# Performance work log

Hardware: AMD Instinct MI355X
Metric: run time of the kernel (lower is better)

The kernel has to match this reference:

```python
import jax, jax.numpy as jnp
import numpy as np

B, N = 8, 16384
DIMS = [3, 64, 128, 1024]  # conv1d(kernel=1) channel sizes: in -> layer_dims -> feat_size
EPS = 1e-5  # BatchNorm1d default eps


def setup_inputs() -> dict:
    key = jax.random.key(0)
    ks = jax.random.split(key, 8)
    inp = {"x": jax.random.normal(ks[0], (B, N, 3), dtype=jnp.float32)}
    for i in range(3):
        cin, cout = DIMS[i], DIMS[i + 1]
        k1, k2 = jax.random.split(ks[i + 1])
        inp[f"W{i}"] = jax.random.normal(k1, (cout, cin), dtype=jnp.float32) * (1.0 / np.sqrt(cin))
        inp[f"b{i}"] = jax.random.normal(k2, (cout,), dtype=jnp.float32) * 0.01
        inp[f"g{i}"] = jnp.ones((cout,), dtype=jnp.float32)   # BN gamma (init 1)
        inp[f"be{i}"] = jnp.zeros((cout,), dtype=jnp.float32)  # BN beta (init 0)
    return inp


def _bn(h, gamma, beta):
    # training-mode BatchNorm1d: stats over batch and point dims, biased variance
    m = h.mean(axis=(0, 1))
    v = h.var(axis=(0, 1))
    return (h - m) * jax.lax.rsqrt(v + EPS) * gamma + beta


def reference(x, W0, b0, g0, be0, W1, b1, g1, be1, W2, b2, g2, be2):
    # pointwise Conv1d (kernel=1) == per-point linear; layout (B, N, C)
    h = jax.nn.relu(_bn(jnp.einsum('bnc,oc->bno', x, W0) + b0, g0, be0))
    local = h  # (B, N, 64) local features
    h = jax.nn.relu(_bn(jnp.einsum('bnc,oc->bno', h, W1) + b1, g1, be1))
    h = _bn(jnp.einsum('bnc,oc->bno', h, W2) + b2, g2, be2)  # no relu on last layer
    gfeat = h.max(axis=1)  # (B, 1024) global max-pool over points
    # concat broadcast global feature with local features -> (B, 1024+64, N) in torch layout
    out = jnp.concatenate(
        [jnp.broadcast_to(gfeat[:, :, None], (B, DIMS[-1], N)), jnp.swapaxes(local, 1, 2)], axis=1)
    return out
```

## Files before the change

kernel.cpp:

```cpp
#include <hip/hip_runtime.h>


#define P_TOT  131072
#define NPTS   16384
#define EPSF   1e-5f

typedef __bf16 bf16x8 __attribute__((ext_vector_type(8)));
typedef float  f32x4  __attribute__((ext_vector_type(4)));

#define H0_OFF   0u
#define H1_OFF   16777216u
#define W1B_OFF  50331648u
#define W2B_OFF  50348032u
#define ST_OFF   50610176u
#define MM_OFF   50662400u

#define S0   0
#define Q0   64
#define S1   128
#define Q1   256
#define S2   384
#define Q2   1408
#define SC0  2432
#define SH0  2496
#define SC1  2560
#define SH1  2688
#define GF   4864
#define STATS_ZERO_N 2432

__device__ __forceinline__ unsigned short f2bf(float f) {
  unsigned u = __builtin_bit_cast(unsigned, f);
  u += 0x7fffu + ((u >> 16) & 1u);
  return (unsigned short)(u >> 16);
}
__device__ __forceinline__ float bf2f(unsigned short s) {
  return __builtin_bit_cast(float, ((unsigned)s) << 16);
}
__device__ __forceinline__ unsigned encf(float f) {
  unsigned u = __builtin_bit_cast(unsigned, f);
  return (u & 0x80000000u) ? ~u : (u | 0x80000000u);
}
__device__ __forceinline__ float decf(unsigned e) {
  unsigned u = (e & 0x80000000u) ? (e & 0x7fffffffu) : ~e;
  return __builtin_bit_cast(float, u);
}
__device__ __forceinline__ uint4 pack8(const float* f) {
  uint4 r;
  r.x = (unsigned)f2bf(f[0]) | ((unsigned)f2bf(f[1]) << 16);
  r.y = (unsigned)f2bf(f[2]) | ((unsigned)f2bf(f[3]) << 16);
  r.z = (unsigned)f2bf(f[4]) | ((unsigned)f2bf(f[5]) << 16);
  r.w = (unsigned)f2bf(f[6]) | ((unsigned)f2bf(f[7]) << 16);
  return r;
}
__device__ __forceinline__ uint4 bnrelu8(uint4 v, const float* sc, const float* sh) {
  unsigned vv[4] = {v.x, v.y, v.z, v.w};
  float f[8];
#pragma unroll
  for (int i = 0; i < 4; ++i) {
    float a = bf2f((unsigned short)(vv[i] & 0xffffu));
    float b = bf2f((unsigned short)(vv[i] >> 16));
    f[2*i]   = fmaxf(fmaf(a, sc[2*i],   sh[2*i]),   0.f);
    f[2*i+1] = fmaxf(fmaf(b, sc[2*i+1], sh[2*i+1]), 0.f);
  }
  return pack8(f);
}

__global__ __launch_bounds__(256) void k_layer0(const float* __restrict__ x,
                                                const float* __restrict__ W0,
                                                const float* __restrict__ W1,
                                                const float* __restrict__ W2,
                                                unsigned short* __restrict__ h0b,
                                                unsigned short* __restrict__ w1b,
                                                unsigned short* __restrict__ w2b,
                                                float* __restrict__ stats,
                                                unsigned* __restrict__ mmx) {
  int t = threadIdx.x;
  if (blockIdx.x >= 2048) {
    int tid = (blockIdx.x - 2048) * 256 + t;
    const int stride = 128 * 256;
    for (int i = tid; i < 1024 * 128; i += stride) w2b[i] = f2bf(W2[i]);
    for (int i = tid; i < 128 * 64;   i += stride) w1b[i] = f2bf(W1[i]);
    for (int i = 128 + tid; i < STATS_ZERO_N; i += stride) stats[i] = 0.f;
    for (int i = tid; i < 8192; i += stride) { mmx[i] = 0u; mmx[8192 + i] = 0xffffffffu; }
    return;
  }
  __shared__ float w0s[192];
  __shared__ float bs[64], bq[64];
  if (t < 192) w0s[t] = W0[t];
  if (t < 64) { bs[t] = 0.f; bq[t] = 0.f; }
  __syncthreads();
  int p  = blockIdx.x * 64 + (t >> 2);
  int cs = (t & 3) * 16;
  float x0 = x[p*3], x1 = x[p*3+1], x2 = x[p*3+2];
  float v[16];
#pragma unroll
  for (int j = 0; j < 16; ++j) {
    int c = cs + j;
    v[j] = x0 * w0s[c*3] + x1 * w0s[c*3+1] + x2 * w0s[c*3+2];
  }
  uint4* dst = (uint4*)(h0b + p*64 + cs);
  dst[0] = pack8(&v[0]);
  dst[1] = pack8(&v[8]);
  int lane = t & 63;
#pragma unroll
  for (int j = 0; j < 16; ++j) {
    float s = v[j], q = v[j]*v[j];
#pragma unroll
    for (int m = 4; m < 64; m <<= 1) { s += __shfl_xor(s, m, 64); q += __shfl_xor(q, m, 64); }
    if (lane < 4) { atomicAdd(&bs[cs + j], s); atomicAdd(&bq[cs + j], q); }
  }
  __syncthreads();
  if (t < 64) { atomicAdd(&stats[S0 + t], bs[t]); atomicAdd(&stats[Q0 + t], bq[t]); }
}

__global__ void k_fin0(const float* __restrict__ g, const float* __restrict__ be,
                       float* __restrict__ stats) {
  int c = threadIdx.x;
  float m = stats[S0 + c] * (1.f / P_TOT);
  float q = stats[Q0 + c] * (1.f / P_TOT);
  float sc = g[c] * rsqrtf(q - m*m + EPSF);
  stats[SC0 + c] = sc;
  stats[SH0 + c] = be[c] - m * sc;
}
__global__ void k_fin1(const float* __restrict__ g, const float* __restrict__ be,
                       float* __restrict__ stats) {
  int c = threadIdx.x;
  float m = stats[S1 + c] * (1.f / P_TOT);
  float q = stats[Q1 + c] * (1.f / P_TOT);
  float sc = g[c] * rsqrtf(q - m*m + EPSF);
  stats[SC1 + c] = sc;
  stats[SH1 + c] = be[c] - m * sc;
}

__global__ __launch_bounds__(512, 2) void k_gemm1(const unsigned short* __restrict__ h0b,
                                                  const unsigned short* __restrict__ w1b,
                                                  unsigned short* __restrict__ h1b,
                                                  float* __restrict__ stats,
                                                  float* __restrict__ out) {
  __shared__ uint4 arrA[128 * 8];
  int t = threadIdx.x, l = t & 63, w = t >> 6;
  int wr = w >> 2, wc = w & 3;
  bf16x8 bfr[2][2];
#pragma unroll
  for (int nn = 0; nn < 2; ++nn)
#pragma unroll
    for (int kk = 0; kk < 2; ++kk) {
      int j  = wc*32 + nn*16 + (l & 15);
      int k0 = kk*32 + (l >> 4) * 8;
      bfr[nn][kk] = __builtin_bit_cast(bf16x8, *(const uint4*)(w1b + j*64 + k0));
    }
  int kc = t & 7;
  float ssc[8], ssh[8];
#pragma unroll
  for (int j = 0; j < 8; ++j) { ssc[j] = stats[SC0 + kc*8 + j]; ssh[j] = stats[SH0 + kc*8 + j]; }
  float runS[2] = {0,0}, runQ[2] = {0,0};
  int pbase0 = blockIdx.x * 256;
  int srow0 = t >> 3, srow1 = 64 + (t >> 3);
  uint4 v0 = *(const uint4*)(h0b + (pbase0 + srow0) * 64 + kc * 8);
  uint4 v1 = *(const uint4*)(h0b + (pbase0 + srow1) * 64 + kc * 8);
  for (int mt = 0; mt < 2; ++mt) {
    int pbase = pbase0 + mt * 128;
    __syncthreads();
    arrA[srow0*8 + (kc ^ (srow0 & 7))] = bnrelu8(v0, ssc, ssh);
    arrA[srow1*8 + (kc ^ (srow1 & 7))] = bnrelu8(v1, ssc, ssh);
    __syncthreads();
    if (mt == 0) {
      v0 = *(const uint4*)(h0b + (pbase0 + 128 + srow0) * 64 + kc * 8);
      v1 = *(const uint4*)(h0b + (pbase0 + 128 + srow1) * 64 + kc * 8);
    }
    f32x4 acc[4][2];
#pragma unroll
    for (int mm = 0; mm < 4; ++mm)
#pragma unroll
      for (int nn = 0; nn < 2; ++nn) acc[mm][nn] = (f32x4){0.f,0.f,0.f,0.f};
#pragma unroll
    for (int kk = 0; kk < 2; ++kk) {
      bf16x8 a[4];
#pragma unroll
      for (int mm = 0; mm < 4; ++mm) {
        int r  = wr*64 + mm*16 + (l & 15);
        int ck = kk*4 + (l >> 4);
        a[mm] = __builtin_bit_cast(bf16x8, arrA[r*8 + (ck ^ (r & 7))]);
      }
#pragma unroll
      for (int mm = 0; mm < 4; ++mm)
#pragma unroll
        for (int nn = 0; nn < 2; ++nn)
          acc[mm][nn] = __builtin_amdgcn_mfma_f32_16x16x32_bf16(a[mm], bfr[nn][kk], acc[mm][nn], 0, 0, 0);
    }
#pragma unroll
    for (int mm = 0; mm < 4; ++mm) {
      int prow = pbase + wr*64 + mm*16 + (l >> 4) * 4;
#pragma unroll
      for (int nn = 0; nn < 2; ++nn) {
        int col = wc*32 + nn*16 + (l & 15);
#pragma unroll
        for (int r = 0; r < 4; ++r) {
          float f = acc[mm][nn][r];
          h1b[(size_t)(prow + r) * 128 + col] = f2bf(f);
          runS[nn] += f;
          runQ[nn] = fmaf(f, f, runQ[nn]);
        }
      }
    }
    {
      int b  = pbase >> 14;
      int n0 = pbase & 16383;
      int c  = t >> 3;
      int seg = t & 7;
      const unsigned short* lds16 = (const unsigned short*)arrA;
      size_t obase = ((size_t)b * 1088 + 1024 + c) * NPTS + n0 + seg * 16;
#pragma unroll
      for (int q = 0; q < 4; ++q) {
        float f[4];
#pragma unroll
        for (int e = 0; e < 4; ++e) {
          int row = seg*16 + q*4 + e;
          f[e] = bf2f(lds16[(row*8 + ((c >> 3) ^ (row & 7)))*8 + (c & 7)]);
        }
        f32x4 o = {f[0], f[1], f[2], f[3]};
        __builtin_nontemporal_store(o, (f32x4*)(out + obase + q*4));
      }
    }
  }
#pragma unroll
  for (int nn = 0; nn < 2; ++nn) {
    float s = runS[nn], q = runQ[nn];
    s += __shfl_xor(s, 16, 64); s += __shfl_xor(s, 32, 64);
    q += __shfl_xor(q, 16, 64); q += __shfl_xor(q, 32, 64);
    if (l < 16) {
      int col = wc*32 + nn*16 + l;
      atomicAdd(&stats[S1 + col], s);
      atomicAdd(&stats[Q1 + col], q);
    }
  }
}

__global__ __launch_bounds__(512, 2) void k_gemm2(const unsigned short* __restrict__ h1b,
                                                  const unsigned short* __restrict__ w2b,
                                                  float* __restrict__ stats,
                                                  unsigned* __restrict__ mmx) {
  __shared__ uint4 arrA[64 * 16];
  int t = threadIdx.x, l = t & 63, w = t >> 6;
  int jw = blockIdx.x * 256 + w * 32;
  int pbase0 = blockIdx.y * 512;
  int bidx = pbase0 >> 14;
  bf16x8 bfr[2][4];
#pragma unroll
  for (int nn = 0; nn < 2; ++nn)
#pragma unroll
    for (int kk = 0; kk < 4; ++kk) {
      int j  = jw + nn*16 + (l & 15);
      int k0 = kk*32 + (l >> 4) * 8;
      bfr[nn][kk] = __builtin_bit_cast(bf16x8, *(const uint4*)(w2b + j*128 + k0));
    }
  int kc = t & 15;
  float ssc[8], ssh[8];
#pragma unroll
  for (int j = 0; j < 8; ++j) { ssc[j] = stats[SC1 + kc*8 + j]; ssh[j] = stats[SH1 + kc*8 + j]; }
  float runS[2] = {0,0}, runQ[2] = {0,0};
  float runMax[2] = {-3.4e38f, -3.4e38f}, runMin[2] = {3.4e38f, 3.4e38f};
  int srow0 = t >> 4, srow1 = 32 + (t >> 4);
  uint4 v0 = *(const uint4*)(h1b + (size_t)(pbase0 + srow0) * 128 + kc * 8);
  uint4 v1 = *(const uint4*)(h1b + (size_t)(pbase0 + srow1) * 128 + kc * 8);
  for (int mt = 0; mt < 8; ++mt) {
    __syncthreads();
    arrA[srow0*16 + (kc ^ (srow0 & 7))] = bnrelu8(v0, ssc, ssh);
    arrA[srow1*16 + (kc ^ (srow1 & 7))] = bnrelu8(v1, ssc, ssh);
    __syncthreads();
    if (mt < 7) {
      int pb = pbase0 + (mt + 1) * 64;
      v0 = *(const uint4*)(h1b + (size_t)(pb + srow0) * 128 + kc * 8);
      v1 = *(const uint4*)(h1b + (size_t)(pb + srow1) * 128 + kc * 8);
    }
    f32x4 acc[4][2];
#pragma unroll
    for (int mm = 0; mm < 4; ++mm)
#pragma unroll
      for (int nn = 0; nn < 2; ++nn) acc[mm][nn] = (f32x4){0.f,0.f,0.f,0.f};
#pragma unroll
    for (int kk = 0; kk < 4; ++kk) {
      bf16x8 a[4];
#pragma unroll
      for (int mm = 0; mm < 4; ++mm) {
        int r  = mm*16 + (l & 15);
        int ck = kk*4 + (l >> 4);
        a[mm] = __builtin_bit_cast(bf16x8, arrA[r*16 + (ck ^ (r & 7))]);
      }
#pragma unroll
      for (int mm = 0; mm < 4; ++mm)
#pragma unroll
        for (int nn = 0; nn < 2; ++nn)
          acc[mm][nn] = __builtin_amdgcn_mfma_f32_16x16x32_bf16(a[mm], bfr[nn][kk], acc[mm][nn], 0, 0, 0);
    }
#pragma unroll
    for (int nn = 0; nn < 2; ++nn)
#pragma unroll
      for (int mm = 0; mm < 4; ++mm)
#pragma unroll
        for (int r = 0; r < 4; ++r) {
          float f = acc[mm][nn][r];
          runS[nn] += f;
          runQ[nn] = fmaf(f, f, runQ[nn]);
          runMax[nn] = fmaxf(runMax[nn], f);
          runMin[nn] = fminf(runMin[nn], f);
        }
  }
#pragma unroll
  for (int nn = 0; nn < 2; ++nn) {
    float s = runS[nn], q = runQ[nn], mx = runMax[nn], mn = runMin[nn];
    s += __shfl_xor(s, 16, 64); s += __shfl_xor(s, 32, 64);
    q += __shfl_xor(q, 16, 64); q += __shfl_xor(q, 32, 64);
    mx = fmaxf(mx, __shfl_xor(mx, 16, 64)); mx = fmaxf(mx, __shfl_xor(mx, 32, 64));
    mn = fminf(mn, __shfl_xor(mn, 16, 64)); mn = fminf(mn, __shfl_xor(mn, 32, 64));
    if (l < 16) {
      int col = jw + nn*16 + l;
      atomicAdd(&stats[S2 + col], s);
      atomicAdd(&stats[Q2 + col], q);
      atomicMax(&mmx[bidx * 1024 + col], encf(mx));
      atomicMin(&mmx[8192 + bidx * 1024 + col], encf(mn));
    }
  }
}

__global__ void k_fin2(const float* __restrict__ g, const float* __restrict__ be,
                       float* __restrict__ stats, const unsigned* __restrict__ mmx) {
  int idx = blockIdx.x * 256 + threadIdx.x;
  int c = idx & 1023, b = idx >> 10;
  float m = stats[S2 + c] * (1.f / P_TOT);
  float q = stats[Q2 + c] * (1.f / P_TOT);
  float sc = g[c] * rsqrtf(q - m*m + EPSF);
  float sh = be[c] - m * sc;
  float mx = decf(mmx[b * 1024 + c]);
  float mn = decf(mmx[8192 + b * 1024 + c]);
  stats[GF + idx] = (sc >= 0.f) ? fmaf(mx, sc, sh) : fmaf(mn, sc, sh);
}

__global__ __launch_bounds__(256) void k_bcast(const float* __restrict__ stats,
                                               float* __restrict__ out) {
  const float* gf = stats + GF;
  int t = threadIdx.x;
#pragma unroll
  for (int rr = 0; rr < 4; ++rr) {
    int row = blockIdx.x * 4 + rr;
    int b = row >> 10, c = row & 1023;
    float v = gf[row];
    f32x4 o = {v, v, v, v};
    float* base = out + ((size_t)b * 1088 + c) * NPTS;
#pragma unroll
    for (int j = 0; j < 16; ++j)
      __builtin_nontemporal_store(o, (f32x4*)(base + (j * 256 + t) * 4));
  }
}

extern "C" void kernel_launch(void* const* d_in, const int* in_sizes, int n_in,
                              void* d_out, int out_size, void* d_ws, size_t ws_size,
                              hipStream_t stream) {
  const float* x   = (const float*)d_in[0];
  const float* W0  = (const float*)d_in[1];
  const float* g0  = (const float*)d_in[3];
  const float* be0 = (const float*)d_in[4];
  const float* W1  = (const float*)d_in[5];
  const float* g1  = (const float*)d_in[7];
  const float* be1 = (const float*)d_in[8];
  const float* W2  = (const float*)d_in[9];
  const float* g2  = (const float*)d_in[11];
  const float* be2 = (const float*)d_in[12];
  float* out = (float*)d_out;
  char* ws = (char*)d_ws;
  unsigned short* h0b = (unsigned short*)(ws + H0_OFF);
  unsigned short* h1b = (unsigned short*)(ws + H1_OFF);
  unsigned short* w1b = (unsigned short*)(ws + W1B_OFF);
  unsigned short* w2b = (unsigned short*)(ws + W2B_OFF);
  float* stats = (float*)(ws + ST_OFF);
  unsigned* mmx = (unsigned*)(ws + MM_OFF);

  k_layer0<<<2176, 256, 0, stream>>>(x, W0, W1, W2, h0b, w1b, w2b, stats, mmx);
  k_fin0  <<<1, 64, 0, stream>>>(g0, be0, stats);
  k_gemm1 <<<512, 512, 0, stream>>>(h0b, w1b, h1b, stats, out);
  k_fin1  <<<1, 128, 0, stream>>>(g1, be1, stats);
  k_gemm2 <<<dim3(4, 256), 512, 0, stream>>>(h1b, w2b, stats, mmx);
  k_fin2  <<<32, 256, 0, stream>>>(g2, be2, stats, mmx);
  k_bcast <<<2048, 256, 0, stream>>>(stats, out);
}
```

Before: 729.4 us.

## Fold BN finalize kernels into consumer kernels and double gemm2 per-block rows

Removes the three tiny BN-finalize launches by having each consumer block compute scale and shift from the raw sums into shared memory, or per row in the broadcast kernel. Separately, gemm2 blocks now cover 1024 points instead of 512, halving the grid along y and doubling loop iterations. The sync placement moves from the top of each loop iteration to the end. This cuts launch gaps and per-block weight-fragment reloads, at the cost of redundant per-block stat computation and fewer blocks in gemm2.

```diff
diff --git a/kernel.cpp b/kernel.cpp
--- a/kernel.cpp
+++ b/kernel.cpp
@@ -21,11 +21,6 @@
 #define Q1   256
 #define S2   384
 #define Q2   1408
-#define SC0  2432
-#define SH0  2496
-#define SC1  2560
-#define SH1  2688
-#define GF   4864
 #define STATS_ZERO_N 2432
 
 __device__ __forceinline__ unsigned short f2bf(float f) {
@@ -113,33 +108,24 @@
   if (t < 64) { atomicAdd(&stats[S0 + t], bs[t]); atomicAdd(&stats[Q0 + t], bq[t]); }
 }
 
-__global__ void k_fin0(const float* __restrict__ g, const float* __restrict__ be,
-                       float* __restrict__ stats) {
-  int c = threadIdx.x;
-  float m = stats[S0 + c] * (1.f / P_TOT);
-  float q = stats[Q0 + c] * (1.f / P_TOT);
-  float sc = g[c] * rsqrtf(q - m*m + EPSF);
-  stats[SC0 + c] = sc;
-  stats[SH0 + c] = be[c] - m * sc;
-}
-__global__ void k_fin1(const float* __restrict__ g, const float* __restrict__ be,
-                       float* __restrict__ stats) {
-  int c = threadIdx.x;
-  float m = stats[S1 + c] * (1.f / P_TOT);
-  float q = stats[Q1 + c] * (1.f / P_TOT);
-  float sc = g[c] * rsqrtf(q - m*m + EPSF);
-  stats[SC1 + c] = sc;
-  stats[SH1 + c] = be[c] - m * sc;
-}
-
 __global__ __launch_bounds__(512, 2) void k_gemm1(const unsigned short* __restrict__ h0b,
                                                   const unsigned short* __restrict__ w1b,
                                                   unsigned short* __restrict__ h1b,
                                                   float* __restrict__ stats,
-                                                  float* __restrict__ out) {
+                                                  float* __restrict__ out,
+                                                  const float* __restrict__ g0,
+                                                  const float* __restrict__ be0) {
   __shared__ uint4 arrA[128 * 8];
+  __shared__ float sc0s[64], sh0s[64];
   int t = threadIdx.x, l = t & 63, w = t >> 6;
   int wr = w >> 2, wc = w & 3;
+  if (t < 64) {
+    float m = stats[S0 + t] * (1.f / P_TOT);
+    float q = stats[Q0 + t] * (1.f / P_TOT);
+    float sc = g0[t] * rsqrtf(q - m*m + EPSF);
+    sc0s[t] = sc;
+    sh0s[t] = be0[t] - m * sc;
+  }
   bf16x8 bfr[2][2];
 #pragma unroll
   for (int nn = 0; nn < 2; ++nn)
@@ -150,17 +136,17 @@
       bfr[nn][kk] = __builtin_bit_cast(bf16x8, *(const uint4*)(w1b + j*64 + k0));
     }
   int kc = t & 7;
-  float ssc[8], ssh[8];
-#pragma unroll
-  for (int j = 0; j < 8; ++j) { ssc[j] = stats[SC0 + kc*8 + j]; ssh[j] = stats[SH0 + kc*8 + j]; }
-  float runS[2] = {0,0}, runQ[2] = {0,0};
   int pbase0 = blockIdx.x * 256;
   int srow0 = t >> 3, srow1 = 64 + (t >> 3);
   uint4 v0 = *(const uint4*)(h0b + (pbase0 + srow0) * 64 + kc * 8);
   uint4 v1 = *(const uint4*)(h0b + (pbase0 + srow1) * 64 + kc * 8);
+  __syncthreads();
+  float ssc[8], ssh[8];
+#pragma unroll
+  for (int j = 0; j < 8; ++j) { ssc[j] = sc0s[kc*8 + j]; ssh[j] = sh0s[kc*8 + j]; }
+  float runS[2] = {0,0}, runQ[2] = {0,0};
   for (int mt = 0; mt < 2; ++mt) {
     int pbase = pbase0 + mt * 128;
-    __syncthreads();
     arrA[srow0*8 + (kc ^ (srow0 & 7))] = bnrelu8(v0, ssc, ssh);
     arrA[srow1*8 + (kc ^ (srow1 & 7))] = bnrelu8(v1, ssc, ssh);
     __syncthreads();
@@ -222,6 +208,7 @@
         __builtin_nontemporal_store(o, (f32x4*)(out + obase + q*4));
       }
     }
+    __syncthreads();
   }
 #pragma unroll
   for (int nn = 0; nn < 2; ++nn) {
@@ -239,12 +226,22 @@
 __global__ __launch_bounds__(512, 2) void k_gemm2(const unsigned short* __restrict__ h1b,
                                                   const unsigned short* __restrict__ w2b,
                                                   float* __restrict__ stats,
-                                                  unsigned* __restrict__ mmx) {
+                                                  unsigned* __restrict__ mmx,
+                                                  const float* __restrict__ g1,
+                                                  const float* __restrict__ be1) {
   __shared__ uint4 arrA[64 * 16];
+  __shared__ float sc1s[128], sh1s[128];
   int t = threadIdx.x, l = t & 63, w = t >> 6;
   int jw = blockIdx.x * 256 + w * 32;
-  int pbase0 = blockIdx.y * 512;
+  int pbase0 = blockIdx.y * 1024;
   int bidx = pbase0 >> 14;
+  if (t < 128) {
+    float m = stats[S1 + t] * (1.f / P_TOT);
+    float q = stats[Q1 + t] * (1.f / P_TOT);
+    float sc = g1[t] * rsqrtf(q - m*m + EPSF);
+    sc1s[t] = sc;
+    sh1s[t] = be1[t] - m * sc;
+  }
   bf16x8 bfr[2][4];
 #pragma unroll
   for (int nn = 0; nn < 2; ++nn)
@@ -255,20 +252,20 @@
       bfr[nn][kk] = __builtin_bit_cast(bf16x8, *(const uint4*)(w2b + j*128 + k0));
     }
   int kc = t & 15;
-  float ssc[8], ssh[8];
-#pragma unroll
-  for (int j = 0; j < 8; ++j) { ssc[j] = stats[SC1 + kc*8 + j]; ssh[j] = stats[SH1 + kc*8 + j]; }
-  float runS[2] = {0,0}, runQ[2] = {0,0};
-  float runMax[2] = {-3.4e38f, -3.4e38f}, runMin[2] = {3.4e38f, 3.4e38f};
   int srow0 = t >> 4, srow1 = 32 + (t >> 4);
   uint4 v0 = *(const uint4*)(h1b + (size_t)(pbase0 + srow0) * 128 + kc * 8);
   uint4 v1 = *(const uint4*)(h1b + (size_t)(pbase0 + srow1) * 128 + kc * 8);
-  for (int mt = 0; mt < 8; ++mt) {
-    __syncthreads();
+  __syncthreads();
+  float ssc[8], ssh[8];
+#pragma unroll
+  for (int j = 0; j < 8; ++j) { ssc[j] = sc1s[kc*8 + j]; ssh[j] = sh1s[kc*8 + j]; }
+  float runS[2] = {0,0}, runQ[2] = {0,0};
+  float runMax[2] = {-3.4e38f, -3.4e38f}, runMin[2] = {3.4e38f, 3.4e38f};
+  for (int mt = 0; mt < 16; ++mt) {
     arrA[srow0*16 + (kc ^ (srow0 & 7))] = bnrelu8(v0, ssc, ssh);
     arrA[srow1*16 + (kc ^ (srow1 & 7))] = bnrelu8(v1, ssc, ssh);
     __syncthreads();
-    if (mt < 7) {
+    if (mt < 15) {
       int pb = pbase0 + (mt + 1) * 64;
       v0 = *(const uint4*)(h1b + (size_t)(pb + srow0) * 128 + kc * 8);
       v1 = *(const uint4*)(h1b + (size_t)(pb + srow1) * 128 + kc * 8);
@@ -305,6 +302,7 @@
           runMax[nn] = fmaxf(runMax[nn], f);
           runMin[nn] = fminf(runMin[nn], f);
         }
+    __syncthreads();
   }
 #pragma unroll
   for (int nn = 0; nn < 2; ++nn) {
@@ -323,28 +321,30 @@
   }
 }
 
-__global__ void k_fin2(const float* __restrict__ g, const float* __restrict__ be,
-                       float* __restrict__ stats, const unsigned* __restrict__ mmx) {
-  int idx = blockIdx.x * 256 + threadIdx.x;
-  int c = idx & 1023, b = idx >> 10;
-  float m = stats[S2 + c] * (1.f / P_TOT);
-  float q = stats[Q2 + c] * (1.f / P_TOT);
-  float sc = g[c] * rsqrtf(q - m*m + EPSF);
-  float sh = be[c] - m * sc;
-  float mx = decf(mmx[b * 1024 + c]);
-  float mn = decf(mmx[8192 + b * 1024 + c]);
-  stats[GF + idx] = (sc >= 0.f) ? fmaf(mx, sc, sh) : fmaf(mn, sc, sh);
-}
-
 __global__ __launch_bounds__(256) void k_bcast(const float* __restrict__ stats,
+                                               const unsigned* __restrict__ mmx,
+                                               const float* __restrict__ g2,
+                                               const float* __restrict__ be2,
                                                float* __restrict__ out) {
-  const float* gf = stats + GF;
+  __shared__ float vrow[4];
   int t = threadIdx.x;
+  if (t < 4) {
+    int row = blockIdx.x * 4 + t;
+    int c = row & 1023, b = row >> 10;
+    float m = stats[S2 + c] * (1.f / P_TOT);
+    float q = stats[Q2 + c] * (1.f / P_TOT);
+    float sc = g2[c] * rsqrtf(q - m*m + EPSF);
+    float sh = be2[c] - m * sc;
+    float mx = decf(mmx[b * 1024 + c]);
+    float mn = decf(mmx[8192 + b * 1024 + c]);
+    vrow[t] = (sc >= 0.f) ? fmaf(mx, sc, sh) : fmaf(mn, sc, sh);
+  }
+  __syncthreads();
 #pragma unroll
   for (int rr = 0; rr < 4; ++rr) {
     int row = blockIdx.x * 4 + rr;
     int b = row >> 10, c = row & 1023;
-    float v = gf[row];
+    float v = vrow[rr];
     f32x4 o = {v, v, v, v};
     float* base = out + ((size_t)b * 1088 + c) * NPTS;
 #pragma unroll
@@ -376,10 +376,7 @@
   unsigned* mmx = (unsigned*)(ws + MM_OFF);
 
   k_layer0<<<2176, 256, 0, stream>>>(x, W0, W1, W2, h0b, w1b, w2b, stats, mmx);
-  k_fin0  <<<1, 64, 0, stream>>>(g0, be0, stats);
-  k_gemm1 <<<512, 512, 0, stream>>>(h0b, w1b, h1b, stats, out);
-  k_fin1  <<<1, 128, 0, stream>>>(g1, be1, stats);
-  k_gemm2 <<<dim3(4, 256), 512, 0, stream>>>(h1b, w2b, stats, mmx);
-  k_fin2  <<<32, 256, 0, stream>>>(g2, be2, stats, mmx);
-  k_bcast <<<2048, 256, 0, stream>>>(stats, out);
-}
+  k_gemm1 <<<512, 512, 0, stream>>>(h0b, w1b, h1b, stats, out, g0, be0);
+  k_gemm2 <<<dim3(4, 128), 512, 0, stream>>>(h1b, w2b, stats, mmx, g1, be1);
+  k_bcast <<<2048, 256, 0, stream>>>(stats, mmx, g2, be2, out);
+}
```

Measured after the change: 719.0 us. Within noise of the previous version (-1.4%).
